# Optimization experiments

Measured on AMD Instinct MI355X. Metric: run time of the kernel, lower is better.

## Reference

```python
import jax, jax.numpy as jnp
import numpy as np

B, S, D, H, F = 4, 1024, 1024, 16, 4096
DH = D // H
EPS = 1e-3  # keras LayerNormalization default epsilon


def _layer_norm(x, g, b):
    mu = jnp.mean(x, axis=-1, keepdims=True)
    var = jnp.mean(jnp.square(x - mu), axis=-1, keepdims=True)
    return (x - mu) * jax.lax.rsqrt(var + EPS) * g + b


def setup_inputs() -> dict:
    key = jax.random.key(0)
    ks = jax.random.split(key, 12)
    p = lambda k, shape: (0.02 * jax.random.normal(k, shape, dtype=jnp.float32))
    inp = {
        "inputs": jax.random.normal(ks[0], (B, S, D), dtype=jnp.float32),
        "paddings": jnp.zeros((B, S), dtype=jnp.float32),
        "attention_bias": jax.random.normal(ks[1], (B, H, S, S), dtype=jnp.float32),
        "attention_mask": jnp.ones((B, S, S), dtype=jnp.float32),
        "ln1_g": jnp.ones((D,), jnp.float32), "ln1_b": jnp.zeros((D,), jnp.float32),
        "wq": p(ks[2], (D, D)), "bq": jnp.zeros((D,), jnp.float32),
        "wk": p(ks[3], (D, D)), "bk": jnp.zeros((D,), jnp.float32),
        "wv": p(ks[4], (D, D)), "bv": jnp.zeros((D,), jnp.float32),
        "wo": p(ks[5], (D, D)), "bo": jnp.zeros((D,), jnp.float32),
        "ln2_g": jnp.ones((D,), jnp.float32), "ln2_b": jnp.zeros((D,), jnp.float32),
        "w1": p(ks[6], (D, F)), "b1": jnp.zeros((F,), jnp.float32),
        "w2": p(ks[7], (F, D)), "b2": jnp.zeros((D,), jnp.float32),
    }
    return inp


def reference(inputs, paddings, attention_bias, attention_mask,
              ln1_g, ln1_b, wq, bq, wk, bk, wv, bv, wo, bo,
              ln2_g, ln2_b, w1, b1, w2, b2):
    # ----- combined mask: [B,S,S] (broadcast over heads) -----
    keep = 1.0 - paddings                           # [B,S]
    pad_mask = keep[:, :, None] * keep[:, None, :]  # [B,T,S]
    mask = attention_mask * pad_mask                # [B,T,S]

    # ----- self-attention on pre-normalized inputs -----
    xn = _layer_norm(inputs, ln1_g, ln1_b)          # [B,S,D]
    q = (xn @ wq + bq).reshape(B, S, H, DH)
    k = (xn @ wk + bk).reshape(B, S, H, DH)
    v = (xn @ wv + bv).reshape(B, S, H, DH)

    logits = jnp.einsum('bthd,bshd->bhts', q, k) / jnp.sqrt(jnp.float32(DH))
    logits = logits + attention_bias - 1e9 * (1.0 - mask[:, None, :, :])
    attn = jax.nn.softmax(logits, axis=-1)          # [B,H,T,S]
    ctx = jnp.einsum('bhts,bshd->bthd', attn, v).reshape(B, S, D)
    atten_out = ctx @ wo + bo + inputs              # residual

    # ----- feed-forward block -----
    yn = _layer_norm(atten_out, ln2_g, ln2_b)
    h = jax.nn.gelu(yn @ w1 + b1, approximate=False)  # keras 'gelu' is exact
    out = atten_out + (h @ w2 + b2)
    out = out * (1.0 - paddings[:, :, None])
    return out
```

## Files before the change

### kernel.cpp

```cpp
#include <hip/hip_runtime.h>
#include <cstdint>
#include <cstddef>

#define B_   4
#define S_   1024
#define D_   1024
#define H_   16
#define DH_  64
#define F_   4096
#define MTOT 4096
#define QKV3 3072
#define KOFF 1024
#define VOFF 2048
#define SMBASE 16.0f

typedef __bf16 bf16x8 __attribute__((ext_vector_type(8)));
typedef float  f32x4  __attribute__((ext_vector_type(4)));

__device__ __forceinline__ unsigned short f2bf(float f){
  uint32_t u = __builtin_bit_cast(uint32_t, f);
  u += 0x7fffu + ((u >> 16) & 1u);
  return (unsigned short)(u >> 16);
}

__device__ __forceinline__ void gload_lds16(const void* g, void* l){
  __builtin_amdgcn_global_load_lds((__attribute__((address_space(1))) void*)(g),
                                   (__attribute__((address_space(3))) void*)(l),
                                   16, 0, 0);
}

__global__ __launch_bounds__(256) void transpose_bf16(const float* __restrict__ W,
                                                      unsigned short* __restrict__ WT,
                                                      int K, int N){
  __shared__ float tile[32][33];
  const int tx = threadIdx.x, ty = threadIdx.y;
  const int n0 = blockIdx.x * 32, k0 = blockIdx.y * 32;
  #pragma unroll
  for (int i = 0; i < 4; ++i)
    tile[ty + i*8][tx] = W[(size_t)(k0 + ty + i*8) * N + n0 + tx];
  __syncthreads();
  #pragma unroll
  for (int i = 0; i < 4; ++i)
    WT[(size_t)(n0 + ty + i*8) * K + k0 + tx] = f2bf(tile[tx][ty + i*8]);
}

__global__ __launch_bounds__(256) void bcat_kernel(const float* __restrict__ bq,
                                                   const float* __restrict__ bk,
                                                   const float* __restrict__ bv,
                                                   float* __restrict__ bqkv){
  const int i = blockIdx.x * 256 + threadIdx.x;
  if (i < QKV3)
    bqkv[i] = (i < 1024) ? bq[i] : (i < 2048) ? bk[i - 1024] : bv[i - 2048];
}

__global__ __launch_bounds__(256) void vtrans(const unsigned short* __restrict__ qkv,
                                              unsigned short* __restrict__ vt){
  __shared__ unsigned short tile[32][33];
  const int tx = threadIdx.x, ty = threadIdx.y;
  const int s0 = blockIdx.x * 32, d0 = blockIdx.y * 32;
  const int bh = blockIdx.z;
  const int b = bh >> 4, hh = bh & 15;
  #pragma unroll
  for (int i = 0; i < 4; ++i)
    tile[ty + i*8][tx] = qkv[(size_t)(b*S_ + s0 + ty + i*8) * QKV3 + VOFF + hh*DH_ + d0 + tx];
  __syncthreads();
  #pragma unroll
  for (int i = 0; i < 4; ++i)
    vt[((size_t)bh*DH_ + d0 + ty + i*8) * S_ + s0 + tx] = tile[tx][ty + i*8];
}

__global__ __launch_bounds__(256) void madd_kernel(const float* __restrict__ amask,
                                                   const float* __restrict__ pad,
                                                   float* __restrict__ madd){
  const int total = B_ * S_ * S_ / 4;
  for (int idx = blockIdx.x * 256 + threadIdx.x; idx < total; idx += gridDim.x * 256){
    const int e0 = idx * 4;
    const int b = e0 >> 20;
    const int t = (e0 >> 10) & (S_ - 1);
    const int s = e0 & (S_ - 1);
    const float kt = 1.0f - pad[b*S_ + t];
    const float4 m = *(const float4*)(amask + e0);
    float4 o;
    o.x = -1e9f * (1.0f - m.x * kt * (1.0f - pad[b*S_ + s + 0]));
    o.y = -1e9f * (1.0f - m.y * kt * (1.0f - pad[b*S_ + s + 1]));
    o.z = -1e9f * (1.0f - m.z * kt * (1.0f - pad[b*S_ + s + 2]));
    o.w = -1e9f * (1.0f - m.w * kt * (1.0f - pad[b*S_ + s + 3]));
    *(float4*)(madd + e0) = o;
  }
}

__global__ __launch_bounds__(256) void ln_kernel(const float* __restrict__ x,
                                                 const float* __restrict__ g,
                                                 const float* __restrict__ b,
                                                 unsigned short* __restrict__ out){
  const int row = blockIdx.x;
  const int tid = threadIdx.x;
  float4 xv = ((const float4*)(x + (size_t)row * D_))[tid];
  float s  = xv.x + xv.y + xv.z + xv.w;
  float s2 = xv.x*xv.x + xv.y*xv.y + xv.z*xv.z + xv.w*xv.w;
  #pragma unroll
  for (int off = 32; off > 0; off >>= 1){
    s  += __shfl_down(s, off);
    s2 += __shfl_down(s2, off);
  }
  __shared__ float ws1[4], ws2[4];
  const int w = tid >> 6, lane = tid & 63;
  if (lane == 0){ ws1[w] = s; ws2[w] = s2; }
  __syncthreads();
  const float tot  = ws1[0] + ws1[1] + ws1[2] + ws1[3];
  const float tot2 = ws2[0] + ws2[1] + ws2[2] + ws2[3];
  const float mean = tot * (1.0f / D_);
  const float var  = tot2 * (1.0f / D_) - mean * mean;
  const float rstd = rsqrtf(var + 1e-3f);
  const int c0 = tid * 4;
  ushort4 o;
  o.x = f2bf((xv.x - mean) * rstd * g[c0+0] + b[c0+0]);
  o.y = f2bf((xv.y - mean) * rstd * g[c0+1] + b[c0+1]);
  o.z = f2bf((xv.z - mean) * rstd * g[c0+2] + b[c0+2]);
  o.w = f2bf((xv.w - mean) * rstd * g[c0+3] + b[c0+3]);
  *(ushort4*)(out + (size_t)row * D_ + c0) = o;
}

template<int EPI, int BM>
__global__ __launch_bounds__(256) void gemm_bt(const unsigned short* __restrict__ A,
                                               const unsigned short* __restrict__ BT,
                                               const float* __restrict__ bias,
                                               const float* __restrict__ resid,
                                               const float* __restrict__ pad,
                                               unsigned short* __restrict__ outB,
                                               float* __restrict__ outF,
                                               int N, int K){
  constexpr int MR = BM / 32;
  constexpr int RA = BM / 32;
  __shared__ unsigned short As[BM * 64];
  __shared__ unsigned short Bs[128 * 64];
  const int tid  = threadIdx.x;
  const int lane = tid & 63, w = tid >> 6;
  const int wr = w >> 1, wc = w & 1;
  const int lm = lane & 15, l4 = lane >> 4;
  const int xsw = (lm & 7) << 3;
  const int m0 = blockIdx.x * BM, n0 = blockIdx.y * 128;

  const int rrow = tid >> 3;
  const int ce   = (((tid & 7) ^ (rrow & 7)) << 3);
  const unsigned short* Asrc = A  + (size_t)(m0 + rrow) * K + ce;
  const unsigned short* Bsrc = BT + (size_t)(n0 + rrow) * K + ce;

  f32x4 acc[MR][4] = {};

  #pragma unroll
  for (int ra = 0; ra < RA; ++ra)
    gload_lds16(Asrc + (size_t)(ra*32) * K, &As[(ra*256 + w*64) * 8]);
  #pragma unroll
  for (int rb = 0; rb < 4; ++rb)
    gload_lds16(Bsrc + (size_t)(rb*32) * K, &Bs[(rb*256 + w*64) * 8]);

  for (int k0 = 0; k0 < K; k0 += 64){
    __syncthreads();

    bf16x8 a[MR][2], bb[4][2];
    #pragma unroll
    for (int m = 0; m < MR; ++m)
      #pragma unroll
      for (int kc = 0; kc < 2; ++kc)
        a[m][kc] = *(const bf16x8*)&As[(wr*(BM/2) + m*16 + lm)*64 + ((kc*32 + l4*8) ^ xsw)];
    #pragma unroll
    for (int n = 0; n < 4; ++n)
      #pragma unroll
      for (int kc = 0; kc < 2; ++kc)
        bb[n][kc] = *(const bf16x8*)&Bs[(wc*64 + n*16 + lm)*64 + ((kc*32 + l4*8) ^ xsw)];

    __syncthreads();

    if (k0 + 64 < K){
      #pragma unroll
      for (int ra = 0; ra < RA; ++ra)
        gload_lds16(Asrc + (size_t)(ra*32) * K + (k0 + 64), &As[(ra*256 + w*64) * 8]);
      #pragma unroll
      for (int rb = 0; rb < 4; ++rb)
        gload_lds16(Bsrc + (size_t)(rb*32) * K + (k0 + 64), &Bs[(rb*256 + w*64) * 8]);
    }

    #pragma unroll
    for (int m = 0; m < MR; ++m)
      #pragma unroll
      for (int n = 0; n < 4; ++n)
        #pragma unroll
        for (int kc = 0; kc < 2; ++kc)
          acc[m][n] = __builtin_amdgcn_mfma_f32_16x16x32_bf16(a[m][kc], bb[n][kc], acc[m][n], 0, 0, 0);
  }

  #pragma unroll
  for (int m = 0; m < MR; ++m){
    #pragma unroll
    for (int n = 0; n < 4; ++n){
      #pragma unroll
      for (int r = 0; r < 4; ++r){
        const int row = m0 + wr*(BM/2) + m*16 + l4*4 + r;
        const int col = n0 + wc*64 + n*16 + lm;
        const size_t idx = (size_t)row * N + col;
        float vv = acc[m][n][r] + bias[col];
        if constexpr (EPI == 0){
          outB[idx] = f2bf(vv);
        } else if constexpr (EPI == 1){
          outF[idx] = vv + resid[idx];
        } else if constexpr (EPI == 2){
          outB[idx] = f2bf(0.5f * vv * (1.0f + erff(vv * 0.70710678118654752f)));
        } else {
          float t = vv + resid[idx];
          outF[idx] = t * (1.0f - pad[row]);
        }
      }
    }
  }
}

__global__ __launch_bounds__(256) void attn_kernel(const unsigned short* __restrict__ qkv,
                                                   const unsigned short* __restrict__ vt,
                                                   const float* __restrict__ abias,
                                                   const float* __restrict__ madd,
                                                   unsigned short* __restrict__ ctx){
  const int bid = blockIdx.x;
  const int id2 = (bid & 7) * 128 + (bid >> 3);
  const int tt = id2 & 15, h = (id2 >> 4) & 15, b = id2 >> 8;
  const int t0 = tt * 64;
  const int tid = threadIdx.x;
  const int lane = tid & 63, w = tid >> 6;
  const int lm = lane & 15, l4 = lane >> 4;
  const int xsw = (lm & 7) << 3;

  __shared__ unsigned short Ks[64 * 64];
  __shared__ unsigned short VTs[64 * 64];
  __shared__ unsigned short Ps[4][16 * 72];

  bf16x8 aq[2];
  {
    const int tg = t0 + w*16 + lm;
    const size_t qb = (size_t)(b*S_ + tg) * QKV3 + h*DH_;
    aq[0] = *(const bf16x8*)&qkv[qb + 0  + l4*8];
    aq[1] = *(const bf16x8*)&qkv[qb + 32 + l4*8];
  }

  const unsigned short* kbase = qkv + (size_t)(b*S_) * QKV3 + KOFF + h*DH_;
  const unsigned short* vbase = vt  + (size_t)((b*H_ + h) * DH_) * S_;
  const float* biasbase = abias + (size_t)((b*H_ + h) * S_ + t0 + w*16 + l4*4) * S_;
  const float* maddbase = madd  + (size_t)(b*S_ + t0 + w*16 + l4*4) * S_;

  const int r_st  = tid >> 3;
  const int ce_st = (((tid & 7) ^ (r_st & 7)) << 3);
  const unsigned short* kst = kbase + (size_t)r_st * QKV3 + ce_st;
  const unsigned short* vst = vbase + (size_t)r_st * S_ + ce_st;

  f32x4 accO[4] = {};
  float lrow[4] = {};

  gload_lds16(kst,                   &Ks[w*512]);
  gload_lds16(kst + (size_t)32*QKV3, &Ks[2048 + w*512]);
  gload_lds16(vst,                   &VTs[w*512]);
  gload_lds16(vst + 32*S_,           &VTs[2048 + w*512]);

  for (int s0 = 0; s0 < S_; s0 += 64){
    __syncthreads();

    float bmv[4][4];
    #pragma unroll
    for (int n = 0; n < 4; ++n){
      const int sg = s0 + n*16 + lm;
      #pragma unroll
      for (int r = 0; r < 4; ++r)
        bmv[n][r] = biasbase[(size_t)r * S_ + sg] + maddbase[(size_t)r * S_ + sg];
    }

    f32x4 accS[4] = {};
    __builtin_amdgcn_s_setprio(1);
    #pragma unroll
    for (int n = 0; n < 4; ++n)
      #pragma unroll
      for (int kc = 0; kc < 2; ++kc){
        bf16x8 bk_ = *(const bf16x8*)&Ks[(n*16 + lm)*64 + ((kc*32 + l4*8) ^ xsw)];
        accS[n] = __builtin_amdgcn_mfma_f32_16x16x32_bf16(aq[kc], bk_, accS[n], 0, 0, 0);
      }
    __builtin_amdgcn_s_setprio(0);

    bf16x8 bvv[4][2];
    #pragma unroll
    for (int n = 0; n < 4; ++n)
      #pragma unroll
      for (int ks = 0; ks < 2; ++ks)
        bvv[n][ks] = *(const bf16x8*)&VTs[(n*16 + lm)*64 + ((ks*32 + l4*8) ^ xsw)];

    __syncthreads();

    if (s0 + 64 < S_){
      gload_lds16(kst + (size_t)(s0 + 64)*QKV3, &Ks[w*512]);
      gload_lds16(kst + (size_t)(s0 + 96)*QKV3, &Ks[2048 + w*512]);
      gload_lds16(vst + (s0 + 64),              &VTs[w*512]);
      gload_lds16(vst + 32*S_ + (s0 + 64),      &VTs[2048 + w*512]);
    }

    float ps[4] = {};
    #pragma unroll
    for (int n = 0; n < 4; ++n){
      #pragma unroll
      for (int r = 0; r < 4; ++r){
        const float pv = __expf(fmaf(accS[n][r], 0.125f, bmv[n][r]) - SMBASE);
        accS[n][r] = pv;
        ps[r] += pv;
      }
    }
    #pragma unroll
    for (int r = 0; r < 4; ++r){
      float s = ps[r];
      s += __shfl_xor(s, 1); s += __shfl_xor(s, 2);
      s += __shfl_xor(s, 4); s += __shfl_xor(s, 8);
      lrow[r] += s;
    }

    #pragma unroll
    for (int n = 0; n < 4; ++n)
      #pragma unroll
      for (int r = 0; r < 4; ++r)
        Ps[w][(l4*4 + r)*72 + n*16 + lm] = f2bf(accS[n][r]);

    __builtin_amdgcn_s_setprio(1);
    #pragma unroll
    for (int ks = 0; ks < 2; ++ks){
      bf16x8 ap = *(const bf16x8*)&Ps[w][lm*72 + ks*32 + l4*8];
      #pragma unroll
      for (int n = 0; n < 4; ++n)
        accO[n] = __builtin_amdgcn_mfma_f32_16x16x32_bf16(ap, bvv[n][ks], accO[n], 0, 0, 0);
    }
    __builtin_amdgcn_s_setprio(0);
  }

  #pragma unroll
  for (int n = 0; n < 4; ++n)
    #pragma unroll
    for (int r = 0; r < 4; ++r){
      const int tg = t0 + w*16 + l4*4 + r;
      ctx[(size_t)(b*S_ + tg) * D_ + h*DH_ + n*16 + lm] = f2bf(accO[n][r] / lrow[r]);
    }
}

extern "C" void kernel_launch(void* const* d_in, const int* in_sizes, int n_in,
                              void* d_out, int out_size, void* d_ws, size_t ws_size,
                              hipStream_t stream){
  (void)in_sizes; (void)n_in; (void)out_size; (void)ws_size;
  const float* x     = (const float*)d_in[0];
  const float* pad   = (const float*)d_in[1];
  const float* abias = (const float*)d_in[2];
  const float* amask = (const float*)d_in[3];
  const float* ln1g  = (const float*)d_in[4];
  const float* ln1b  = (const float*)d_in[5];
  const float* wq    = (const float*)d_in[6];
  const float* bq    = (const float*)d_in[7];
  const float* wk    = (const float*)d_in[8];
  const float* bk    = (const float*)d_in[9];
  const float* wv    = (const float*)d_in[10];
  const float* bv    = (const float*)d_in[11];
  const float* wo    = (const float*)d_in[12];
  const float* bo    = (const float*)d_in[13];
  const float* ln2g  = (const float*)d_in[14];
  const float* ln2b  = (const float*)d_in[15];
  const float* w1    = (const float*)d_in[16];
  const float* b1    = (const float*)d_in[17];
  const float* w2    = (const float*)d_in[18];
  const float* b2    = (const float*)d_in[19];
  float* out = (float*)d_out;

  char* p = (char*)d_ws;
  auto take = [&](size_t bytes){ void* r = (void*)p; p += bytes; return r; };
  unsigned short* xn   = (unsigned short*)take((size_t)MTOT * D_ * 2);
  unsigned short* qkv  = (unsigned short*)take((size_t)MTOT * QKV3 * 2);
  unsigned short* ctx  = (unsigned short*)take((size_t)MTOT * D_ * 2);
  unsigned short* yn   = (unsigned short*)take((size_t)MTOT * D_ * 2);
  unsigned short* hb   = (unsigned short*)take((size_t)MTOT * F_ * 2);
  float*          ao   = (float*)take((size_t)MTOT * D_ * 4);
  unsigned short* wqkvT= (unsigned short*)take((size_t)QKV3 * D_ * 2);
  unsigned short* woT  = (unsigned short*)take((size_t)D_ * D_ * 2);
  unsigned short* w1T  = (unsigned short*)take((size_t)D_ * F_ * 2);
  unsigned short* w2T  = (unsigned short*)take((size_t)D_ * F_ * 2);
  float*          bqkv = (float*)take((size_t)QKV3 * 4);
  unsigned short* vtb  = xn;
  float*          madd = (float*)hb;

  const dim3 tb(32, 8);
  transpose_bf16<<<dim3(D_/32, D_/32), tb, 0, stream>>>(wq, wqkvT,                   D_, D_);
  transpose_bf16<<<dim3(D_/32, D_/32), tb, 0, stream>>>(wk, wqkvT + (size_t)D_*D_,   D_, D_);
  transpose_bf16<<<dim3(D_/32, D_/32), tb, 0, stream>>>(wv, wqkvT + (size_t)2*D_*D_, D_, D_);
  transpose_bf16<<<dim3(D_/32, D_/32), tb, 0, stream>>>(wo, woT, D_, D_);
  transpose_bf16<<<dim3(F_/32, D_/32), tb, 0, stream>>>(w1, w1T, D_, F_);
  transpose_bf16<<<dim3(D_/32, F_/32), tb, 0, stream>>>(w2, w2T, F_, D_);

  bcat_kernel<<<12, 256, 0, stream>>>(bq, bk, bv, bqkv);
  madd_kernel<<<2048, 256, 0, stream>>>(amask, pad, madd);

  ln_kernel<<<MTOT, 256, 0, stream>>>(x, ln1g, ln1b, xn);

  gemm_bt<0,128><<<dim3(MTOT/128, QKV3/128), 256, 0, stream>>>(xn, wqkvT, bqkv, nullptr, nullptr, qkv, nullptr, QKV3, D_);

  vtrans<<<dim3(S_/32, DH_/32, B_*H_), tb, 0, stream>>>(qkv, vtb);

  attn_kernel<<<dim3(16*H_*B_), 256, 0, stream>>>(qkv, vtb, abias, madd, ctx);

  gemm_bt<1,64><<<dim3(MTOT/64, D_/128), 256, 0, stream>>>(ctx, woT, bo, x, nullptr, nullptr, ao, D_, D_);

  ln_kernel<<<MTOT, 256, 0, stream>>>(ao, ln2g, ln2b, yn);

  gemm_bt<2,128><<<dim3(MTOT/128, F_/128), 256, 0, stream>>>(yn, w1T, b1, nullptr, nullptr, hb, nullptr, F_, D_);

  gemm_bt<3,64><<<dim3(MTOT/64, D_/128), 256, 0, stream>>>(hb, w2T, b2, ao, pad, nullptr, out, D_, F_);
}
```

Measured before the change: 325.0 us.

## Merge prep kernels and prefetch attention bias one tile ahead

Folds the six weight transposes and the bias concatenation into one launch, and merges the V transpose with the mask-add precompute into a second launch, which cuts kernel launch overhead and tail idle time. Inside the attention kernel, bias plus mask for the next 64-column tile is loaded one iteration early into double-buffered registers, so global load latency overlaps with the current tile's MFMA and softmax work. The cost is higher register pressure in the attention loop and a manually unrolled two-step body.

```diff
diff --git a/kernel.cpp b/kernel.cpp
--- a/kernel.cpp
+++ b/kernel.cpp
@@ -29,12 +29,39 @@
                                    16, 0, 0);
 }
 
-__global__ __launch_bounds__(256) void transpose_bf16(const float* __restrict__ W,
-                                                      unsigned short* __restrict__ WT,
-                                                      int K, int N){
+__global__ __launch_bounds__(256) void prep_weights(const float* __restrict__ wq,
+                                                    const float* __restrict__ wk,
+                                                    const float* __restrict__ wv,
+                                                    const float* __restrict__ wo,
+                                                    const float* __restrict__ w1,
+                                                    const float* __restrict__ w2,
+                                                    const float* __restrict__ bq,
+                                                    const float* __restrict__ bk,
+                                                    const float* __restrict__ bv,
+                                                    unsigned short* __restrict__ wqkvT,
+                                                    unsigned short* __restrict__ woT,
+                                                    unsigned short* __restrict__ w1T,
+                                                    unsigned short* __restrict__ w2T,
+                                                    float* __restrict__ bqkv){
   __shared__ float tile[32][33];
+  const int bid = blockIdx.x;
   const int tx = threadIdx.x, ty = threadIdx.y;
-  const int n0 = blockIdx.x * 32, k0 = blockIdx.y * 32;
+  const float* W; unsigned short* WT; int K, N, n0, k0;
+  if (bid < 3072){
+    W  = (bid < 1024) ? wq : (bid < 2048) ? wk : wv;
+    WT = wqkvT + (size_t)(bid >> 10) * D_ * D_;
+    K = D_; N = D_;
+    const int t = bid & 1023; n0 = (t & 31) * 32; k0 = (t >> 5) * 32;
+  } else if (bid < 4096){
+    W = wo; WT = woT; K = D_; N = D_;
+    const int t = bid - 3072; n0 = (t & 31) * 32; k0 = (t >> 5) * 32;
+  } else if (bid < 8192){
+    W = w1; WT = w1T; K = D_; N = F_;
+    const int t = bid - 4096; n0 = (t & 127) * 32; k0 = (t >> 7) * 32;
+  } else {
+    W = w2; WT = w2T; K = F_; N = D_;
+    const int t = bid - 8192; n0 = (t & 31) * 32; k0 = (t >> 5) * 32;
+  }
   #pragma unroll
   for (int i = 0; i < 4; ++i)
     tile[ty + i*8][tx] = W[(size_t)(k0 + ty + i*8) * N + n0 + tx];
@@ -42,50 +69,49 @@
   #pragma unroll
   for (int i = 0; i < 4; ++i)
     WT[(size_t)(n0 + ty + i*8) * K + k0 + tx] = f2bf(tile[tx][ty + i*8]);
-}
-
-__global__ __launch_bounds__(256) void bcat_kernel(const float* __restrict__ bq,
-                                                   const float* __restrict__ bk,
-                                                   const float* __restrict__ bv,
-                                                   float* __restrict__ bqkv){
-  const int i = blockIdx.x * 256 + threadIdx.x;
-  if (i < QKV3)
+  if (bid < 12){
+    const int i = bid*256 + ty*32 + tx;
     bqkv[i] = (i < 1024) ? bq[i] : (i < 2048) ? bk[i - 1024] : bv[i - 2048];
-}
-
-__global__ __launch_bounds__(256) void vtrans(const unsigned short* __restrict__ qkv,
-                                              unsigned short* __restrict__ vt){
-  __shared__ unsigned short tile[32][33];
-  const int tx = threadIdx.x, ty = threadIdx.y;
-  const int s0 = blockIdx.x * 32, d0 = blockIdx.y * 32;
-  const int bh = blockIdx.z;
-  const int b = bh >> 4, hh = bh & 15;
-  #pragma unroll
-  for (int i = 0; i < 4; ++i)
-    tile[ty + i*8][tx] = qkv[(size_t)(b*S_ + s0 + ty + i*8) * QKV3 + VOFF + hh*DH_ + d0 + tx];
-  __syncthreads();
-  #pragma unroll
-  for (int i = 0; i < 4; ++i)
-    vt[((size_t)bh*DH_ + d0 + ty + i*8) * S_ + s0 + tx] = tile[tx][ty + i*8];
-}
-
-__global__ __launch_bounds__(256) void madd_kernel(const float* __restrict__ amask,
-                                                   const float* __restrict__ pad,
-                                                   float* __restrict__ madd){
-  const int total = B_ * S_ * S_ / 4;
-  for (int idx = blockIdx.x * 256 + threadIdx.x; idx < total; idx += gridDim.x * 256){
-    const int e0 = idx * 4;
-    const int b = e0 >> 20;
-    const int t = (e0 >> 10) & (S_ - 1);
-    const int s = e0 & (S_ - 1);
-    const float kt = 1.0f - pad[b*S_ + t];
-    const float4 m = *(const float4*)(amask + e0);
-    float4 o;
-    o.x = -1e9f * (1.0f - m.x * kt * (1.0f - pad[b*S_ + s + 0]));
-    o.y = -1e9f * (1.0f - m.y * kt * (1.0f - pad[b*S_ + s + 1]));
-    o.z = -1e9f * (1.0f - m.z * kt * (1.0f - pad[b*S_ + s + 2]));
-    o.w = -1e9f * (1.0f - m.w * kt * (1.0f - pad[b*S_ + s + 3]));
-    *(float4*)(madd + e0) = o;
+  }
+}
+
+__global__ __launch_bounds__(256) void mid_prep(const unsigned short* __restrict__ qkv,
+                                                unsigned short* __restrict__ vt,
+                                                const float* __restrict__ amask,
+                                                const float* __restrict__ pad,
+                                                float* __restrict__ madd){
+  const int bid = blockIdx.x;
+  if (bid < 4096){
+    __shared__ unsigned short tile[32][33];
+    const int tx = threadIdx.x, ty = threadIdx.y;
+    const int s0 = (bid & 31) * 32;
+    const int d0 = ((bid >> 5) & 1) * 32;
+    const int bh = bid >> 6;
+    const int b = bh >> 4, hh = bh & 15;
+    #pragma unroll
+    for (int i = 0; i < 4; ++i)
+      tile[ty + i*8][tx] = qkv[(size_t)(b*S_ + s0 + ty + i*8) * QKV3 + VOFF + hh*DH_ + d0 + tx];
+    __syncthreads();
+    #pragma unroll
+    for (int i = 0; i < 4; ++i)
+      vt[((size_t)bh*DH_ + d0 + ty + i*8) * S_ + s0 + tx] = tile[tx][ty + i*8];
+  } else {
+    const int tid = threadIdx.y*32 + threadIdx.x;
+    const int total = B_ * S_ * S_ / 4;
+    for (int idx = (bid - 4096)*256 + tid; idx < total; idx += 2048*256){
+      const int e0 = idx * 4;
+      const int b = e0 >> 20;
+      const int t = (e0 >> 10) & (S_ - 1);
+      const int s = e0 & (S_ - 1);
+      const float kt = 1.0f - pad[b*S_ + t];
+      const float4 m = *(const float4*)(amask + e0);
+      float4 o;
+      o.x = -1e9f * (1.0f - m.x * kt * (1.0f - pad[b*S_ + s + 0]));
+      o.y = -1e9f * (1.0f - m.y * kt * (1.0f - pad[b*S_ + s + 1]));
+      o.z = -1e9f * (1.0f - m.z * kt * (1.0f - pad[b*S_ + s + 2]));
+      o.w = -1e9f * (1.0f - m.w * kt * (1.0f - pad[b*S_ + s + 3]));
+      *(float4*)(madd + e0) = o;
+    }
   }
 }
 
@@ -253,22 +279,30 @@
 
   f32x4 accO[4] = {};
   float lrow[4] = {};
-
+  float bmA[4][4], bmB[4][4];
+
+  #pragma unroll
+  for (int n = 0; n < 4; ++n){
+    const int sg = n*16 + lm;
+    #pragma unroll
+    for (int r = 0; r < 4; ++r)
+      bmA[n][r] = biasbase[(size_t)r * S_ + sg] + maddbase[(size_t)r * S_ + sg];
+  }
   gload_lds16(kst,                   &Ks[w*512]);
   gload_lds16(kst + (size_t)32*QKV3, &Ks[2048 + w*512]);
   gload_lds16(vst,                   &VTs[w*512]);
   gload_lds16(vst + 32*S_,           &VTs[2048 + w*512]);
 
-  for (int s0 = 0; s0 < S_; s0 += 64){
+  auto step = [&](int s0, float (&cur)[4][4], float (&nxt)[4][4]){
     __syncthreads();
 
-    float bmv[4][4];
+    const int sn = (s0 + 64 < S_) ? (s0 + 64) : s0;
     #pragma unroll
     for (int n = 0; n < 4; ++n){
-      const int sg = s0 + n*16 + lm;
+      const int sg = sn + n*16 + lm;
       #pragma unroll
       for (int r = 0; r < 4; ++r)
-        bmv[n][r] = biasbase[(size_t)r * S_ + sg] + maddbase[(size_t)r * S_ + sg];
+        nxt[n][r] = biasbase[(size_t)r * S_ + sg] + maddbase[(size_t)r * S_ + sg];
     }
 
     f32x4 accS[4] = {};
@@ -303,7 +337,7 @@
     for (int n = 0; n < 4; ++n){
       #pragma unroll
       for (int r = 0; r < 4; ++r){
-        const float pv = __expf(fmaf(accS[n][r], 0.125f, bmv[n][r]) - SMBASE);
+        const float pv = __expf(fmaf(accS[n][r], 0.125f, cur[n][r]) - SMBASE);
         accS[n][r] = pv;
         ps[r] += pv;
       }
@@ -331,6 +365,12 @@
         accO[n] = __builtin_amdgcn_mfma_f32_16x16x32_bf16(ap, bvv[n][ks], accO[n], 0, 0, 0);
     }
     __builtin_amdgcn_s_setprio(0);
+  };
+
+  #pragma unroll 1
+  for (int s0 = 0; s0 < S_; s0 += 128){
+    step(s0,      bmA, bmB);
+    step(s0 + 64, bmB, bmA);
   }
 
   #pragma unroll
@@ -385,21 +425,15 @@
   float*          madd = (float*)hb;
 
   const dim3 tb(32, 8);
-  transpose_bf16<<<dim3(D_/32, D_/32), tb, 0, stream>>>(wq, wqkvT,                   D_, D_);
-  transpose_bf16<<<dim3(D_/32, D_/32), tb, 0, stream>>>(wk, wqkvT + (size_t)D_*D_,   D_, D_);
-  transpose_bf16<<<dim3(D_/32, D_/32), tb, 0, stream>>>(wv, wqkvT + (size_t)2*D_*D_, D_, D_);
-  transpose_bf16<<<dim3(D_/32, D_/32), tb, 0, stream>>>(wo, woT, D_, D_);
-  transpose_bf16<<<dim3(F_/32, D_/32), tb, 0, stream>>>(w1, w1T, D_, F_);
-  transpose_bf16<<<dim3(D_/32, F_/32), tb, 0, stream>>>(w2, w2T, F_, D_);
-
-  bcat_kernel<<<12, 256, 0, stream>>>(bq, bk, bv, bqkv);
-  madd_kernel<<<2048, 256, 0, stream>>>(amask, pad, madd);
+
+  prep_weights<<<12288, tb, 0, stream>>>(wq, wk, wv, wo, w1, w2, bq, bk, bv,
+                                         wqkvT, woT, w1T, w2T, bqkv);
 
   ln_kernel<<<MTOT, 256, 0, stream>>>(x, ln1g, ln1b, xn);
 
   gemm_bt<0,128><<<dim3(MTOT/128, QKV3/128), 256, 0, stream>>>(xn, wqkvT, bqkv, nullptr, nullptr, qkv, nullptr, QKV3, D_);
 
-  vtrans<<<dim3(S_/32, DH_/32, B_*H_), tb, 0, stream>>>(qkv, vtb);
+  mid_prep<<<6144, tb, 0, stream>>>(qkv, vtb, amask, pad, madd);
 
   attn_kernel<<<dim3(16*H_*B_), 256, 0, stream>>>(qkv, vtb, abias, madd, ctx);
 
```

Result: faster. 304.7 us (-6.2%).
